# Performance work log

Hardware: AMD Instinct MI355X
Metric: run time of the kernel (lower is better)

## Reference

```python
import jax, jax.numpy as jnp
import numpy as np

B = 16384       # batch size
P = 2           # fixed pooling factor per bag (offsets are arange * P)
NTAB = 26       # number of sparse feature tables
NROWS = 100000  # rows per embedding table
D = 128         # embedding dim == ln_bot[-1]
LN_BOT = [13, 512, 256, 128]
LN_TOP = [479, 1024, 512, 256, 1]


def setup_inputs() -> dict:
    key = jax.random.key(0)
    ks = jax.random.split(key, 32)
    inp = {}
    inp['dense_x'] = jax.random.normal(ks[0], (B, LN_BOT[0]), dtype=jnp.float32)
    # offsets: uniform stride-P bags (EmbeddingBag offsets)
    inp['lS_o'] = jnp.broadcast_to(jnp.arange(B, dtype=jnp.int64) * P, (NTAB, B))
    inp['lS_i'] = jax.random.randint(ks[1], (NTAB, B * P), 0, NROWS, dtype=jnp.int64)
    # embedding tables, uniform(-sqrt(1/n), sqrt(1/n))
    bound = float(np.sqrt(1.0 / NROWS))
    inp['emb_tables'] = jax.random.uniform(ks[2], (NTAB, NROWS, D), dtype=jnp.float32,
                                           minval=-bound, maxval=bound)
    # bot MLP params (He-style scaled normal)
    ki = 3
    for i in range(len(LN_BOT) - 1):
        n, m = LN_BOT[i], LN_BOT[i + 1]
        inp[f'bw{i}'] = jax.random.normal(ks[ki], (m, n), dtype=jnp.float32) * np.sqrt(2.0 / (m + n)); ki += 1
        inp[f'bb{i}'] = jax.random.normal(ks[ki], (m,), dtype=jnp.float32) * np.sqrt(1.0 / m); ki += 1
    for i in range(len(LN_TOP) - 1):
        n, m = LN_TOP[i], LN_TOP[i + 1]
        inp[f'tw{i}'] = jax.random.normal(ks[ki], (m, n), dtype=jnp.float32) * np.sqrt(2.0 / (m + n)); ki += 1
        inp[f'tb{i}'] = jax.random.normal(ks[ki], (m,), dtype=jnp.float32) * np.sqrt(1.0 / m); ki += 1
    return inp


def _mlp(x, Ws, bs, sigmoid_layer):
    for i, (W, b) in enumerate(zip(Ws, bs)):
        x = x @ W.T + b
        x = jax.nn.sigmoid(x) if i == sigmoid_layer else jax.nn.relu(x)
    return x


def reference(dense_x, lS_o, lS_i, emb_tables,
              bw0, bb0, bw1, bb1, bw2, bb2,
              tw0, tb0, tw1, tb1, tw2, tb2, tw3, tb3):
    # bot MLP (sigmoid_bot = -1 -> all ReLU)
    x = _mlp(dense_x, [bw0, bw1, bw2], [bb0, bb1, bb2], sigmoid_layer=-1)  # [B, D]

    # multi-table EmbeddingBag sum pooling. Offsets (lS_o) are uniform stride-P
    # arange bags, so sum pooling is a gather + reshape + sum over P.
    def pool_one(table, idx):
        return table[idx].reshape(B, P, D).sum(axis=1)  # [B, D]
    ly = jax.vmap(pool_one)(emb_tables, lS_i)  # [NTAB, B, D]

    # dot interaction (arch_interaction_itself=False -> strict lower triangle)
    T = jnp.concatenate([x[:, None, :], jnp.transpose(ly, (1, 0, 2))], axis=1)  # [B, 27, D]
    Z = jnp.einsum('bid,bjd->bij', T, T)  # [B, 27, 27]
    ni = NTAB + 1
    li, lj = jnp.tril_indices(ni, k=-1)
    Zflat = Z[:, li, lj]  # [B, 351]
    R = jnp.concatenate([x, Zflat], axis=1)  # [B, 479]

    # top MLP (sigmoid at last layer, sigmoid_top = 3)
    p = _mlp(R, [tw0, tw1, tw2, tw3], [tb0, tb1, tb2, tb3], sigmoid_layer=3)
    return p  # [B, 1]
```

## Files before the change

kernel.cpp:

```cpp
#include <hip/hip_runtime.h>
#include <hip/hip_bf16.h>
#include <math.h>

#define BATCH 16384
#define NTAB 26
#define DIM 128
#define NROWS 100000

typedef short bf16x8 __attribute__((ext_vector_type(8)));
typedef float f32x4 __attribute__((ext_vector_type(4)));
typedef float f32x16 __attribute__((ext_vector_type(16)));

__device__ __forceinline__ ushort f2b(float f) {
  union { float f; unsigned u; } c; c.f = f;
  unsigned r = (c.u + 0x7fffu + ((c.u >> 16) & 1u)) >> 16;
  return (ushort)r;
}
__device__ __forceinline__ float b2f(ushort u) {
  union { unsigned u; float f; } c; c.u = (unsigned)u << 16;
  return c.f;
}

__device__ __forceinline__ void gload_lds16(const void* g, void* l) {
  __builtin_amdgcn_global_load_lds(
      (const __attribute__((address_space(1))) void*)g,
      (__attribute__((address_space(3))) void*)l, 16, 0, 0);
}

__global__ __launch_bounds__(256) void cvt_all_kernel(
    const float* __restrict__ bw1, const float* __restrict__ bw2,
    const float* __restrict__ tw0, const float* __restrict__ tw1,
    const float* __restrict__ tw2,
    ushort* __restrict__ o1, ushort* __restrict__ o2, ushort* __restrict__ o3,
    ushort* __restrict__ o4, ushort* __restrict__ o5) {
  int i = blockIdx.x * 256 + threadIdx.x;
  switch (blockIdx.y) {
    case 0: if (i < 256 * 512) o1[i] = f2b(bw1[i]); break;
    case 1: if (i < 128 * 256) o2[i] = f2b(bw2[i]); break;
    case 2: if (i < 1024 * 512) {
      int r = i >> 9, c = i & 511;
      o3[i] = (c < 479) ? f2b(tw0[(size_t)r * 479 + c]) : (ushort)0;
    } break;
    case 3: if (i < 512 * 1024) o4[i] = f2b(tw1[i]); break;
    case 4: if (i < 256 * 512) o5[i] = f2b(tw2[i]); break;
  }
}

__global__ __launch_bounds__(256) void bot0_kernel(const float* __restrict__ x,
    const float* __restrict__ W, const float* __restrict__ bias, ushort* __restrict__ y) {
  int b = blockIdx.x >> 1;
  int m = ((blockIdx.x & 1) << 8) | threadIdx.x;
  const float* xr = x + (size_t)b * 13;
  const float* wr = W + (size_t)m * 13;
  float acc = bias[m];
#pragma unroll
  for (int k = 0; k < 13; k++) acc = fmaf(xr[k], wr[k], acc);
  y[(size_t)b * 512 + m] = f2b(fmaxf(acc, 0.f));
}

__global__ __launch_bounds__(256) void embint_kernel(
    const float* __restrict__ tables, const int* __restrict__ lS_i,
    const ushort* __restrict__ xb, ushort* __restrict__ R) {
  __shared__ ushort Tls[4][32 * 128];
  const int wave = threadIdx.x >> 6, lane = threadIdx.x & 63;
  const int b = blockIdx.x * 4 + wave;
  char* tl = (char*)Tls[wave];

  *(uint*)(tl + lane * 4) = *(const uint*)(xb + (size_t)b * 128 + lane * 2);
#pragma unroll
  for (int r = 27; r < 32; r++)
    *(uint*)(tl + r * 256 + ((lane * 4) ^ ((r & 7) << 4))) = 0;
#pragma unroll 4
  for (int t = 0; t < NTAB; t++) {
    const int* idx = lS_i + ((size_t)t << 15) + (b << 1);
    int i0 = idx[0], i1 = idx[1];
    float2 v0 = ((const float2*)(tables + ((size_t)t * NROWS + i0) * DIM))[lane];
    float2 v1 = ((const float2*)(tables + ((size_t)t * NROWS + i1) * DIM))[lane];
    ushort2 s; s.x = f2b(v0.x + v1.x); s.y = f2b(v0.y + v1.y);
    int row = t + 1;
    *(uint*)(tl + row * 256 + ((lane * 4) ^ ((row & 7) << 4))) = *(uint*)&s;
  }
  __syncthreads();

  const int row = lane & 31;
  const int khb = (lane >> 5) * 16;
  const int swz = (row & 7) << 4;
  f32x16 z = {};
#pragma unroll
  for (int ks = 0; ks < 8; ks++) {
    bf16x8 a = *(const bf16x8*)(tl + row * 256 + ((ks * 32 + khb) ^ swz));
    z = __builtin_amdgcn_mfma_f32_32x32x16_bf16(a, a, z, 0, 0, 0);
  }

  ushort* Rb = R + (size_t)b * 512;
  *(uint*)(Rb + lane * 2) = *(const uint*)(tl + lane * 4);
  if (lane < 33) Rb[479 + lane] = 0;
  const int j = lane & 31;
  const int rb4 = (lane >> 5) * 4;
#pragma unroll
  for (int r = 0; r < 16; r++) {
    int i = (r & 3) + 8 * (r >> 2) + rb4;
    if (i <= 26 && j < i) Rb[DIM + (i * (i - 1)) / 2 + j] = f2b(z[r]);
  }
}

#define SLOT_BYTES 49152
template <int ACT>
__global__ __launch_bounds__(512, 2) void gemm256_kernel(
    const ushort* __restrict__ A, const ushort* __restrict__ W,
    const float* __restrict__ bias, ushort* __restrict__ C, int K, int ldc) {
  __shared__ char lds[3 * SLOT_BYTES];
  const int tid = threadIdx.x;
  const int lane = tid & 63, wid = tid >> 6;
  const int wm = wid >> 2, wn = wid & 3;
  const int m0 = blockIdx.y * 256, n0 = blockIdx.x * 128;
  const int NK = K >> 6;

  const int srow = tid >> 3;
  const int scolb = (tid & 7) << 4;

#pragma unroll
  for (int kt = 0; kt < 2; kt++) {
    char* As = lds + kt * SLOT_BYTES;
    char* Bs = As + 32768;
    const int k0 = kt * 64;
#pragma unroll
    for (int i = 0; i < 4; i++) {
      int row = i * 64 + srow;
      int colb = scolb ^ ((row & 7) << 4);
      gload_lds16(A + (size_t)(m0 + row) * K + k0 + (colb >> 1), As + i * 8192 + wid * 1024);
    }
#pragma unroll
    for (int i = 0; i < 2; i++) {
      int row = i * 64 + srow;
      int colb = scolb ^ ((row & 7) << 4);
      gload_lds16(W + (size_t)(n0 + row) * K + k0 + (colb >> 1), Bs + i * 8192 + wid * 1024);
    }
  }

  f32x4 acc[8][2] = {};
  const int fr = lane & 15;
  const int fkb = (lane >> 4) * 16;

  for (int kt = 0; kt < NK; kt++) {
    if (kt + 1 < NK) { asm volatile("s_waitcnt vmcnt(6)" ::: "memory"); }
    else             { asm volatile("s_waitcnt vmcnt(0)" ::: "memory"); }
    __builtin_amdgcn_sched_barrier(0);
    __builtin_amdgcn_s_barrier();
    __builtin_amdgcn_sched_barrier(0);

    const char* As = lds + (kt % 3) * SLOT_BYTES;
    const char* Bs = As + 32768;

    bf16x8 a[2][8], b[2][2];
#pragma unroll
    for (int kh = 0; kh < 2; kh++) {
#pragma unroll
      for (int mf = 0; mf < 8; mf++) {
        int row = wm * 128 + mf * 16 + fr;
        int colb = (kh * 64 + fkb) ^ ((row & 7) << 4);
        a[kh][mf] = *(const bf16x8*)(As + row * 128 + colb);
      }
#pragma unroll
      for (int nf = 0; nf < 2; nf++) {
        int row = wn * 32 + nf * 16 + fr;
        int colb = (kh * 64 + fkb) ^ ((row & 7) << 4);
        b[kh][nf] = *(const bf16x8*)(Bs + row * 128 + colb);
      }
    }

    if (kt + 2 < NK) {
      char* Ad = lds + ((kt + 2) % 3) * SLOT_BYTES;
      char* Bd = Ad + 32768;
      const int k0 = (kt + 2) * 64;
#pragma unroll
      for (int i = 0; i < 4; i++) {
        int row = i * 64 + srow;
        int colb = scolb ^ ((row & 7) << 4);
        gload_lds16(A + (size_t)(m0 + row) * K + k0 + (colb >> 1), Ad + i * 8192 + wid * 1024);
      }
#pragma unroll
      for (int i = 0; i < 2; i++) {
        int row = i * 64 + srow;
        int colb = scolb ^ ((row & 7) << 4);
        gload_lds16(W + (size_t)(n0 + row) * K + k0 + (colb >> 1), Bd + i * 8192 + wid * 1024);
      }
    }

    __builtin_amdgcn_s_setprio(1);
#pragma unroll
    for (int kh = 0; kh < 2; kh++)
#pragma unroll
      for (int mf = 0; mf < 8; mf++)
#pragma unroll
        for (int nf = 0; nf < 2; nf++)
          acc[mf][nf] = __builtin_amdgcn_mfma_f32_16x16x32_bf16(a[kh][mf], b[kh][nf], acc[mf][nf], 0, 0, 0);
    __builtin_amdgcn_s_setprio(0);
  }

  const int cr = lane & 15, rh = (lane >> 4) * 4;
#pragma unroll
  for (int nf = 0; nf < 2; nf++) {
    int n = n0 + wn * 32 + nf * 16 + cr;
    float bs = bias[n];
#pragma unroll
    for (int mf = 0; mf < 8; mf++) {
      int mb = m0 + wm * 128 + mf * 16 + rh;
#pragma unroll
      for (int r = 0; r < 4; r++) {
        float v = acc[mf][nf][r] + bs;
        if (ACT) v = fmaxf(v, 0.f);
        C[(size_t)(mb + r) * ldc + n] = f2b(v);
      }
    }
  }
}

template <int ACT>
__global__ __launch_bounds__(256) void gemm_bf16_kernel(
    const ushort* __restrict__ A, const ushort* __restrict__ W,
    const float* __restrict__ bias, ushort* __restrict__ C, int K, int ldc) {
  __shared__ ushort As[128 * 32];
  __shared__ ushort Bs[128 * 32];
  const int tid = threadIdx.x;
  const int lane = tid & 63, wave = tid >> 6;
  const int m0 = blockIdx.y * 128, n0 = blockIdx.x * 128;
  const int wr = wave >> 1, wc = wave & 1;

  const int srow = lane >> 2;
  const int skp = (lane & 3) * 8;
  const ushort* Ag = A + (size_t)(m0 + wave * 16 + srow) * K + skp;
  const ushort* Wg = W + (size_t)(n0 + wave * 16 + srow) * K + skp;
  ushort* AsW = &As[(wave * 16) * 32];
  ushort* BsW = &Bs[(wave * 16) * 32];

  f32x4 acc[4][4] = {};
  const int fr = lane & 15;
  const int fk = (lane >> 4) * 8;

  for (int k0 = 0; k0 < K; k0 += 32) {
    gload_lds16(Ag + k0, AsW);
    gload_lds16(Ag + (size_t)64 * K + k0, AsW + 64 * 32);
    gload_lds16(Wg + k0, BsW);
    gload_lds16(Wg + (size_t)64 * K + k0, BsW + 64 * 32);
    __syncthreads();
    bf16x8 a[4], b[4];
#pragma unroll
    for (int i = 0; i < 4; i++) {
      a[i] = *(const bf16x8*)&As[(wr * 64 + i * 16 + fr) * 32 + fk];
      b[i] = *(const bf16x8*)&Bs[(wc * 64 + i * 16 + fr) * 32 + fk];
    }
#pragma unroll
    for (int i = 0; i < 4; i++)
#pragma unroll
      for (int j = 0; j < 4; j++)
        acc[i][j] = __builtin_amdgcn_mfma_f32_16x16x32_bf16(a[i], b[j], acc[i][j], 0, 0, 0);
    __syncthreads();
  }

  const int col_l = lane & 15, row_h = (lane >> 4) * 4;
#pragma unroll
  for (int j = 0; j < 4; j++) {
    int n = n0 + wc * 64 + j * 16 + col_l;
    float bs = bias[n];
#pragma unroll
    for (int i = 0; i < 4; i++) {
      int mbase = m0 + wr * 64 + i * 16 + row_h;
#pragma unroll
      for (int r = 0; r < 4; r++) {
        float v = acc[i][j][r] + bs;
        if (ACT) v = fmaxf(v, 0.f);
        C[(size_t)(mbase + r) * ldc + n] = f2b(v);
      }
    }
  }
}

__global__ __launch_bounds__(256) void final_kernel(const ushort* __restrict__ A,
    const float* __restrict__ w, const float* __restrict__ bias, float* __restrict__ out) {
  int row = blockIdx.x * 4 + (threadIdx.x >> 6);
  int lane = threadIdx.x & 63;
  ushort4 a4 = ((const ushort4*)(A + (size_t)row * 256))[lane];
  float4 wv = ((const float4*)w)[lane];
  float s = b2f(a4.x) * wv.x + b2f(a4.y) * wv.y + b2f(a4.z) * wv.z + b2f(a4.w) * wv.w;
#pragma unroll
  for (int off = 32; off >= 1; off >>= 1) s += __shfl_xor(s, off);
  if (lane == 0) out[row] = 1.f / (1.f + expf(-(s + bias[0])));
}

extern "C" void kernel_launch(void* const* d_in, const int* in_sizes, int n_in,
                              void* d_out, int out_size, void* d_ws, size_t ws_size,
                              hipStream_t stream) {
  const float* dense_x = (const float*)d_in[0];
  const int* lS_i = (const int*)d_in[2];
  const float* emb = (const float*)d_in[3];
  const float* bw0 = (const float*)d_in[4];
  const float* bb0 = (const float*)d_in[5];
  const float* bw1 = (const float*)d_in[6];
  const float* bb1 = (const float*)d_in[7];
  const float* bw2 = (const float*)d_in[8];
  const float* bb2 = (const float*)d_in[9];
  const float* tw0 = (const float*)d_in[10];
  const float* tb0 = (const float*)d_in[11];
  const float* tw1 = (const float*)d_in[12];
  const float* tb1 = (const float*)d_in[13];
  const float* tw2 = (const float*)d_in[14];
  const float* tb2 = (const float*)d_in[15];
  const float* tw3 = (const float*)d_in[16];
  const float* tb3 = (const float*)d_in[17];
  float* out = (float*)d_out;

  char* w = (char*)d_ws;
  ushort* xb  = (ushort*)w; w += (size_t)BATCH * 128 * 2;
  ushort* x1  = (ushort*)w; w += (size_t)BATCH * 512 * 2;
  ushort* x2  = (ushort*)w; w += (size_t)BATCH * 256 * 2;
  ushort* R   = (ushort*)w; w += (size_t)BATCH * 512 * 2;
  ushort* t1  = (ushort*)w; w += (size_t)BATCH * 1024 * 2;
  ushort* wb1 = (ushort*)w; w += 256 * 512 * 2;
  ushort* wb2 = (ushort*)w; w += 128 * 256 * 2;
  ushort* wt0 = (ushort*)w; w += 1024 * 512 * 2;
  ushort* wt1 = (ushort*)w; w += 512 * 1024 * 2;
  ushort* wt2 = (ushort*)w; w += 256 * 512 * 2;
  ushort* t2 = x1;
  ushort* t3 = x2;

  cvt_all_kernel<<<dim3(2048, 5), 256, 0, stream>>>(bw1, bw2, tw0, tw1, tw2,
                                                    wb1, wb2, wt0, wt1, wt2);

  bot0_kernel<<<BATCH * 2, 256, 0, stream>>>(dense_x, bw0, bb0, x1);
  gemm_bf16_kernel<1><<<dim3(2, BATCH / 128), 256, 0, stream>>>(x1, wb1, bb1, x2, 512, 256);
  gemm_bf16_kernel<1><<<dim3(1, BATCH / 128), 256, 0, stream>>>(x2, wb2, bb2, xb, 256, 128);

  embint_kernel<<<BATCH / 4, 256, 0, stream>>>(emb, lS_i, xb, R);

  gemm256_kernel<1><<<dim3(1024 / 128, BATCH / 256), 512, 0, stream>>>(R,  wt0, tb0, t1, 512, 1024);
  gemm256_kernel<1><<<dim3(512 / 128,  BATCH / 256), 512, 0, stream>>>(t1, wt1, tb1, t2, 1024, 512);
  gemm_bf16_kernel<1><<<dim3(2, BATCH / 128), 256, 0, stream>>>(t2, wt2, tb2, t3, 512, 256);
  final_kernel<<<BATCH / 4, 256, 0, stream>>>(t3, tw3, tb3, out);
}
```

Before: 226.2 us.

## Split GEMM K-tile into interleaved half-phases and swizzle workgroups across XCDs

Remaps the workgroup ID so consecutive tiles land on the same XCD, which is meant to improve L2 reuse of A and W tiles. The main loop is also split into two k-halves. Each half loads its own fragments, issues part of the next-stage global-to-LDS copies, then synchronises with extra barriers before running its MFMAs. This interleaves memory issue with compute in ping-pong style and lowers register pressure from holding both halves of the fragments. The cost is more barriers per iteration and a risk of stalls if the warps fall out of phase.

```diff
diff --git a/kernel.cpp b/kernel.cpp
--- a/kernel.cpp
+++ b/kernel.cpp
@@ -113,7 +113,13 @@
   const int tid = threadIdx.x;
   const int lane = tid & 63, wid = tid >> 6;
   const int wm = wid >> 2, wn = wid & 3;
-  const int m0 = blockIdx.y * 256, n0 = blockIdx.x * 128;
+
+  const int nwg = gridDim.x * gridDim.y;
+  const int orig = blockIdx.y * gridDim.x + blockIdx.x;
+  const int q = nwg >> 3, r8 = nwg & 7;
+  const int xcd = orig & 7, pos = orig >> 3;
+  const int swzid = (xcd < r8 ? xcd * (q + 1) : r8 * (q + 1) + (xcd - r8) * q) + pos;
+  const int m0 = (swzid / gridDim.x) * 256, n0 = (swzid % gridDim.x) * 128;
   const int NK = K >> 6;
 
   const int srow = tid >> 3;
@@ -151,51 +157,56 @@
 
     const char* As = lds + (kt % 3) * SLOT_BYTES;
     const char* Bs = As + 32768;
-
-    bf16x8 a[2][8], b[2][2];
+    char* Ad = lds + ((kt + 2) % 3) * SLOT_BYTES;
+    char* Bd = Ad + 32768;
+    const int k2 = (kt + 2) * 64;
+    const bool do_stage = (kt + 2 < NK);
+
 #pragma unroll
     for (int kh = 0; kh < 2; kh++) {
+      bf16x8 a[8], b[2];
 #pragma unroll
       for (int mf = 0; mf < 8; mf++) {
         int row = wm * 128 + mf * 16 + fr;
         int colb = (kh * 64 + fkb) ^ ((row & 7) << 4);
-        a[kh][mf] = *(const bf16x8*)(As + row * 128 + colb);
+        a[mf] = *(const bf16x8*)(As + row * 128 + colb);
       }
 #pragma unroll
       for (int nf = 0; nf < 2; nf++) {
         int row = wn * 32 + nf * 16 + fr;
         int colb = (kh * 64 + fkb) ^ ((row & 7) << 4);
-        b[kh][nf] = *(const bf16x8*)(Bs + row * 128 + colb);
-      }
-    }
-
-    if (kt + 2 < NK) {
-      char* Ad = lds + ((kt + 2) % 3) * SLOT_BYTES;
-      char* Bd = Ad + 32768;
-      const int k0 = (kt + 2) * 64;
-#pragma unroll
-      for (int i = 0; i < 4; i++) {
-        int row = i * 64 + srow;
-        int colb = scolb ^ ((row & 7) << 4);
-        gload_lds16(A + (size_t)(m0 + row) * K + k0 + (colb >> 1), Ad + i * 8192 + wid * 1024);
-      }
-#pragma unroll
-      for (int i = 0; i < 2; i++) {
-        int row = i * 64 + srow;
-        int colb = scolb ^ ((row & 7) << 4);
-        gload_lds16(W + (size_t)(n0 + row) * K + k0 + (colb >> 1), Bd + i * 8192 + wid * 1024);
-      }
-    }
-
-    __builtin_amdgcn_s_setprio(1);
-#pragma unroll
-    for (int kh = 0; kh < 2; kh++)
+        b[nf] = *(const bf16x8*)(Bs + row * 128 + colb);
+      }
+      if (do_stage) {
+#pragma unroll
+        for (int i = kh * 2; i < kh * 2 + 2; i++) {
+          int row = i * 64 + srow;
+          int colb = scolb ^ ((row & 7) << 4);
+          gload_lds16(A + (size_t)(m0 + row) * K + k2 + (colb >> 1), Ad + i * 8192 + wid * 1024);
+        }
+        {
+          int row = kh * 64 + srow;
+          int colb = scolb ^ ((row & 7) << 4);
+          gload_lds16(W + (size_t)(n0 + row) * K + k2 + (colb >> 1), Bd + kh * 8192 + wid * 1024);
+        }
+      }
+      __builtin_amdgcn_sched_barrier(0);
+      __builtin_amdgcn_s_barrier();
+      asm volatile("s_waitcnt lgkmcnt(0)" ::: "memory");
+      __builtin_amdgcn_sched_barrier(0);
+      __builtin_amdgcn_s_setprio(1);
 #pragma unroll
       for (int mf = 0; mf < 8; mf++)
 #pragma unroll
         for (int nf = 0; nf < 2; nf++)
-          acc[mf][nf] = __builtin_amdgcn_mfma_f32_16x16x32_bf16(a[kh][mf], b[kh][nf], acc[mf][nf], 0, 0, 0);
-    __builtin_amdgcn_s_setprio(0);
+          acc[mf][nf] = __builtin_amdgcn_mfma_f32_16x16x32_bf16(a[mf], b[nf], acc[mf][nf], 0, 0, 0);
+      __builtin_amdgcn_s_setprio(0);
+      if (kh == 0) {
+        __builtin_amdgcn_sched_barrier(0);
+        __builtin_amdgcn_s_barrier();
+        __builtin_amdgcn_sched_barrier(0);
+      }
+    }
   }
 
   const int cr = lane & 15, rh = (lane >> 4) * 4;
```

Result: no change. 222.8 us (-1.5%).
